# Performance work log

Measured on AMD Instinct MI355X. Metric: run time of the kernel, lower is better.

## Reference

```python
import jax, jax.numpy as jnp
import numpy as np
from jax import lax

DIM, HEADS, WS = 256, 8, 8
B, H, W = 2, 192, 192


def conv1x1(x, w, b):
    # x: (b,c,h,w), w: (o,c)
    return jnp.einsum('bchw,oc->bohw', x, w) + b[None, :, None, None]


def dwconv3x3(x, w, b):
    # w: (C,1,3,3), zeros padding (padding_mode='zeros')
    y = lax.conv_general_dilated(x, w, (1, 1), ((1, 1), (1, 1)),
                                 dimension_numbers=('NCHW', 'OIHW', 'NCHW'),
                                 feature_group_count=x.shape[1])
    return y + b[None, :, None, None]


def window_split(qkv):
    # (b, 3*heads*c, H, W) -> (3, b*h1*w1, heads, c, ws*ws)
    b, C3, h, w = qkv.shape
    c = C3 // (3 * HEADS)
    h1, w1 = h // WS, w // WS
    t = qkv.reshape(b, 3, HEADS, c, h1, WS, w1, WS)
    t = t.transpose(1, 0, 4, 6, 2, 3, 5, 7)  # (3,b,h1,w1,heads,c,ws,ws)
    return t.reshape(3, b * h1 * w1, HEADS, c, WS * WS)


def window_merge(o, b, h, w):
    # (b*h1*w1, heads, c, ws*ws) -> (b, heads*c, h, w)
    h1, w1 = h // WS, w // WS
    c = o.shape[2]
    t = o.reshape(b, h1, w1, HEADS, c, WS, WS)
    t = t.transpose(0, 3, 4, 1, 5, 2, 6)  # (b,heads,c,h1,ws,w1,ws)
    return t.reshape(b, HEADS * c, h, w)


def l2norm(x):
    n = jnp.linalg.norm(x, axis=-1, keepdims=True)
    return x / jnp.maximum(n, 1e-12)


def setup_inputs() -> dict:
    key = jax.random.key(0)
    ks = jax.random.split(key, 16)
    s = 0.02
    return {
        'x': jax.random.normal(ks[0], (B, DIM, H, W), jnp.float32),
        'x2': jax.random.normal(ks[1], (B, DIM, H, W), jnp.float32),
        'w_qkv': jax.random.normal(ks[2], (3 * DIM, DIM), jnp.float32) * s,
        'b_qkv': jnp.zeros((3 * DIM,), jnp.float32),
        'w_dw': jax.random.normal(ks[3], (3 * DIM, 1, 3, 3), jnp.float32) * s,
        'b_dw': jnp.zeros((3 * DIM,), jnp.float32),
        'w_qkv2': jax.random.normal(ks[4], (3 * DIM, DIM), jnp.float32) * s,
        'b_qkv2': jnp.zeros((3 * DIM,), jnp.float32),
        'w_dw2': jax.random.normal(ks[5], (3 * DIM, 1, 3, 3), jnp.float32) * s,
        'b_dw2': jnp.zeros((3 * DIM,), jnp.float32),
        'temp': jnp.ones((HEADS, 1, 1), jnp.float32) / np.sqrt(DIM).astype(np.float32),
        'w_proj': jax.random.normal(ks[6], (DIM, DIM), jnp.float32) * s,
        'b_proj': jnp.zeros((DIM,), jnp.float32),
    }


def reference(x, x2, w_qkv, b_qkv, w_dw, b_dw, w_qkv2, b_qkv2, w_dw2, b_dw2,
              temp, w_proj, b_proj):
    b, _, h, w = x.shape
    qkv = dwconv3x3(conv1x1(x, w_qkv, b_qkv), w_dw, b_dw)
    qkv2 = dwconv3x3(conv1x1(x2, w_qkv2, b_qkv2), w_dw2, b_dw2)
    # H,W divisible by window_size -> check_image_size is a no-op
    q, k, v = window_split(qkv)       # each (Bw, heads, c, N)
    q2, k2, v2 = window_split(qkv2)
    q, k = l2norm(q), l2norm(k)
    q2, k2 = l2norm(q2), l2norm(k2)
    # channel attention (cs='channel'): scores are (c x c) per window/head
    cross = jnp.einsum('whcn,whdn->whcd', q, k2) * temp  # q @ k2^T
    cross = jax.nn.softmax(cross, axis=-1)
    cross_out = jnp.einsum('whcd,whdn->whcn', cross, v2)
    out = window_merge(cross_out, b, h, w)
    return conv1x1(out, w_proj, b_proj)
```

## Files before the change

kernel.cpp:

```cpp
#include <hip/hip_runtime.h>
#include <stdint.h>

typedef unsigned short u16;
typedef __attribute__((ext_vector_type(4))) unsigned short u16x4;
typedef __attribute__((ext_vector_type(8))) short bf16x8;
typedef __attribute__((ext_vector_type(4))) float f32x4;

#define PTOT 36864
#define WIMG 192

__device__ __forceinline__ float bf2f(u16 h) {
    union { uint32_t u; float f; } v; v.u = ((uint32_t)h) << 16; return v.f;
}
__device__ __forceinline__ u16 f2bf(float f) {
    union { float f; uint32_t u; } v; v.f = f;
    uint32_t u = v.u;
    return (u16)((u + 0x7FFFu + ((u >> 16) & 1u)) >> 16);
}

#define ASYNC_COPY16(gp, lp)                                                     \
    __builtin_amdgcn_global_load_lds(                                            \
        (const __attribute__((address_space(1))) void*)(gp),                     \
        (__attribute__((address_space(3))) void*)(lp), 16, 0, 0)

__global__ __launch_bounds__(256) void k_transpose(const float* __restrict__ x,
                                                   u16* __restrict__ xt) {
    __shared__ u16 tile[32][33];
    const int tx = threadIdx.x, ty = threadIdx.y;
    const int p0 = blockIdx.x * 32, c0 = blockIdx.y * 32, b = blockIdx.z;
    const float* src = x + (size_t)b * 256 * PTOT;
    u16* dst = xt + (size_t)b * PTOT * 256;
#pragma unroll
    for (int k = 0; k < 4; ++k) {
        int c = c0 + ty + k * 8;
        tile[ty + k * 8][tx] = f2bf(src[(size_t)c * PTOT + p0 + tx]);
    }
    __syncthreads();
#pragma unroll
    for (int k = 0; k < 4; ++k) {
        int p = p0 + ty + k * 8;
        dst[(size_t)p * 256 + c0 + tx] = tile[tx][ty + k * 8];
    }
}

__global__ void k_f2bf(const float* __restrict__ src, u16* __restrict__ dst, int n) {
    int i = blockIdx.x * 256 + threadIdx.x;
    if (i < n) dst[i] = f2bf(src[i]);
}

template <bool OUT_F32>
__global__ __launch_bounds__(256) void k_gemm(const u16* __restrict__ A,
                                              const u16* __restrict__ Bt,
                                              void* __restrict__ Cout,
                                              const float* __restrict__ bias,
                                              int M) {
    __shared__ u16 As[128 * 32];
    __shared__ u16 Bs[128 * 32];
    const int tid = threadIdx.x;
    const int lane = tid & 63;
    const int wave = tid >> 6;
    const int wr = wave >> 1, wc = wave & 1;
    const int nb = blockIdx.x, mb = blockIdx.y, b = blockIdx.z;

    const u16* Ab = A + (size_t)(mb * 128) * 256;
    const u16* Bb = Bt + ((size_t)b * PTOT + (size_t)nb * 128) * 256;

    const int lrow = lane >> 2;
    const int lcol = (lane & 3) * 8;
    const int lr = lane & 15;
    const int lk = lane >> 4;

    f32x4 acc[4][4];
#pragma unroll
    for (int m = 0; m < 4; ++m)
#pragma unroll
        for (int n = 0; n < 4; ++n) acc[m][n] = (f32x4)0.f;

    for (int k0 = 0; k0 < 256; k0 += 32) {
        __syncthreads();
        const int i0 = wave * 2;
#pragma unroll
        for (int ii = 0; ii < 2; ++ii) {
            const int i = i0 + ii;
            ASYNC_COPY16(Ab + (size_t)(i * 16 + lrow) * 256 + k0 + lcol,
                         As + i * 16 * 32);
            ASYNC_COPY16(Bb + (size_t)(i * 16 + lrow) * 256 + k0 + lcol,
                         Bs + i * 16 * 32);
        }
        __syncthreads();
        const bf16x8* Asv = (const bf16x8*)As;
        const bf16x8* Bsv = (const bf16x8*)Bs;
        bf16x8 afr[4], bfr[4];
#pragma unroll
        for (int m = 0; m < 4; ++m)
            afr[m] = Asv[(wr * 64 + m * 16 + lr) * 4 + lk];
#pragma unroll
        for (int n = 0; n < 4; ++n)
            bfr[n] = Bsv[(wc * 64 + n * 16 + lr) * 4 + lk];
#pragma unroll
        for (int m = 0; m < 4; ++m)
#pragma unroll
            for (int n = 0; n < 4; ++n)
                acc[m][n] = __builtin_amdgcn_mfma_f32_16x16x32_bf16(
                    afr[m], bfr[n], acc[m][n], 0, 0, 0);
    }

    const int cr = (lane >> 4) * 4;
    const int cc = lane & 15;
#pragma unroll
    for (int m = 0; m < 4; ++m) {
#pragma unroll
        for (int j = 0; j < 4; ++j) {
            const int row = mb * 128 + wr * 64 + m * 16 + cr + j;
            const float bv = bias[row];
            const size_t rbase =
                ((size_t)b * M + row) * PTOT + (size_t)nb * 128 + wc * 64 + cc;
#pragma unroll
            for (int n = 0; n < 4; ++n) {
                const float v = acc[m][n][j] + bv;
                if (OUT_F32)
                    ((float*)Cout)[rbase + n * 16] = v;
                else
                    ((u16*)Cout)[rbase + n * 16] = f2bf(v);
            }
        }
    }
}

__global__ __launch_bounds__(256) void k_dwconv(const u16* __restrict__ in,
                                                u16* __restrict__ out,
                                                const float* __restrict__ w,
                                                const float* __restrict__ bias,
                                                int C) {
    const int vec = blockIdx.x * 256 + threadIdx.x;
    const int ch = blockIdx.y, b = blockIdx.z;
    const int yg = vec / 24, xv = vec - yg * 24;
    const int y0 = yg * 2;
    const size_t base = ((size_t)(b * C + ch)) * PTOT;
    const float* wc9 = w + ch * 9;

    float p[4][10];
#pragma unroll
    for (int r = 0; r < 4; ++r) {
        const int yy = y0 - 1 + r;
        if ((unsigned)yy >= (unsigned)WIMG) {
#pragma unroll
            for (int i = 0; i < 10; ++i) p[r][i] = 0.f;
        } else {
            const u16* row = in + base + (size_t)yy * WIMG + xv * 8;
            const bf16x8 cv = *(const bf16x8*)row;
            p[r][0] = (xv > 0) ? bf2f(row[-1]) : 0.f;
            p[r][9] = (xv < 23) ? bf2f(row[8]) : 0.f;
#pragma unroll
            for (int i = 0; i < 8; ++i) p[r][i + 1] = bf2f((u16)cv[i]);
        }
    }

    const float bv = bias[ch];
#pragma unroll
    for (int r = 0; r < 2; ++r) {
        float acc[8];
#pragma unroll
        for (int i = 0; i < 8; ++i) acc[i] = bv;
#pragma unroll
        for (int dy = 0; dy < 3; ++dy) {
            const float wa = wc9[dy * 3], wbv = wc9[dy * 3 + 1], wcv = wc9[dy * 3 + 2];
            const float* pr = p[r + dy];
#pragma unroll
            for (int i = 0; i < 8; ++i)
                acc[i] += wa * pr[i] + wbv * pr[i + 1] + wcv * pr[i + 2];
        }
        bf16x8 ov;
#pragma unroll
        for (int i = 0; i < 8; ++i) ov[i] = (short)f2bf(acc[i]);
        *(bf16x8*)(out + base + (size_t)(y0 + r) * WIMG + xv * 8) = ov;
    }
}

__global__ __launch_bounds__(256) void k_attn(const u16* __restrict__ q,
                                              const u16* __restrict__ kv,
                                              const float* __restrict__ temp,
                                              u16* __restrict__ outt) {
    __shared__ __align__(16) u16 lds[29280];
    u16* Q = lds;
    u16* K = lds + 9248;
    u16* VT = lds + 18496;
    float* IQ = (float*)(lds + 28768);
    float* IK = (float*)(lds + 29024);
    float* SS = (float*)(lds + 9248);
    u16* P = lds;

    const int tid = threadIdx.x;
    const int lane = tid & 63;
    const int wv = tid >> 6;
    const int h = blockIdx.y, b = blockIdx.z;
    const int wy = blockIdx.x / 6, wxg = blockIdx.x % 6;
    const int px0 = wxg * 32;

    const size_t qbase = ((size_t)b * 256 + h * 32) * PTOT;
    const size_t kbase = ((size_t)b * 512 + h * 32) * PTOT;
    const size_t vbase = kbase + (size_t)256 * PTOT;

#pragma unroll
    for (int it = 0; it < 4; ++it) {
        const int L = it * 256 + tid;
        const int c = L >> 5, rem = L & 31, rr = rem >> 2, w = rem & 3;
        const size_t gp = (size_t)(wy * 8 + rr) * WIMG + px0 + w * 8;
        bf16x8 qv = *(const bf16x8*)(q + qbase + (size_t)c * PTOT + gp);
        bf16x8 kvv = *(const bf16x8*)(kv + kbase + (size_t)c * PTOT + gp);
        bf16x8 vv = *(const bf16x8*)(kv + vbase + (size_t)c * PTOT + gp);
        *(bf16x8*)(Q + w * 2312 + c * 72 + rr * 8) = qv;
        *(bf16x8*)(K + w * 2312 + c * 72 + rr * 8) = kvv;
        u16* vt = VT + w * 2568 + rr * 8 * 40 + c;
#pragma unroll
        for (int j = 0; j < 8; ++j) vt[j * 40] = (u16)vv[j];
    }
    __syncthreads();

    {
        const int w = (tid >> 5) & 3, c = tid & 31;
        const u16* row = (tid < 128 ? Q : K) + w * 2312 + c * 72;
        float s = 0.f;
#pragma unroll
        for (int j = 0; j < 8; ++j) {
            bf16x8 v = *(const bf16x8*)(row + j * 8);
#pragma unroll
            for (int i = 0; i < 8; ++i) { float f = bf2f((u16)v[i]); s += f * f; }
        }
        const float inv = 1.f / fmaxf(sqrtf(s), 1e-12f);
        (tid < 128 ? IQ : IK)[w * 32 + c] = inv;
    }
    __syncthreads();

    {
        const int lr = lane & 15, lk = lane >> 4;
        f32x4 s00 = (f32x4)0.f, s01 = (f32x4)0.f, s10 = (f32x4)0.f, s11 = (f32x4)0.f;
        const u16* Qw = Q + wv * 2312 + lk * 8;
        const u16* Kw = K + wv * 2312 + lk * 8;
#pragma unroll
        for (int kb = 0; kb < 2; ++kb) {
            bf16x8 a0 = *(const bf16x8*)(Qw + lr * 72 + kb * 32);
            bf16x8 a1 = *(const bf16x8*)(Qw + (16 + lr) * 72 + kb * 32);
            bf16x8 b0 = *(const bf16x8*)(Kw + lr * 72 + kb * 32);
            bf16x8 b1 = *(const bf16x8*)(Kw + (16 + lr) * 72 + kb * 32);
            s00 = __builtin_amdgcn_mfma_f32_16x16x32_bf16(a0, b0, s00, 0, 0, 0);
            s01 = __builtin_amdgcn_mfma_f32_16x16x32_bf16(a0, b1, s01, 0, 0, 0);
            s10 = __builtin_amdgcn_mfma_f32_16x16x32_bf16(a1, b0, s10, 0, 0, 0);
            s11 = __builtin_amdgcn_mfma_f32_16x16x32_bf16(a1, b1, s11, 0, 0, 0);
        }
        float* srow = SS + wv * 1156;
        const int cr = lk * 4, cc = lr;
#pragma unroll
        for (int j = 0; j < 4; ++j) {
            srow[(cr + j) * 36 + cc] = s00[j];
            srow[(cr + j) * 36 + 16 + cc] = s01[j];
            srow[(16 + cr + j) * 36 + cc] = s10[j];
            srow[(16 + cr + j) * 36 + 16 + cc] = s11[j];
        }
    }
    __syncthreads();

    if (tid < 128) {
        const int w = tid >> 5, c = tid & 31;
        const float* srow = SS + w * 1156 + c * 36;
        const float* ik = IK + w * 32;
        const float iq = IQ[w * 32 + c] * temp[h];
        float sv[32];
        float mx = -1e30f;
#pragma unroll
        for (int d = 0; d < 32; ++d) {
            sv[d] = srow[d] * ik[d] * iq;
            mx = fmaxf(mx, sv[d]);
        }
        float sum = 0.f;
#pragma unroll
        for (int d = 0; d < 32; ++d) {
            sv[d] = __expf(sv[d] - mx);
            sum += sv[d];
        }
        const float inv = 1.f / sum;
        u16* prow = P + w * 2312 + c * 40;
#pragma unroll
        for (int ch = 0; ch < 4; ++ch) {
            bf16x8 pv;
#pragma unroll
            for (int i = 0; i < 8; ++i) pv[i] = (short)f2bf(sv[ch * 8 + i] * inv);
            *(bf16x8*)(prow + ch * 8) = pv;
        }
    }
    __syncthreads();

    {
        const int lr = lane & 15, lk = lane >> 4;
        bf16x8 pa0 = *(const bf16x8*)(P + wv * 2312 + lr * 40 + lk * 8);
        bf16x8 pa1 = *(const bf16x8*)(P + wv * 2312 + (16 + lr) * 40 + lk * 8);
        f32x4 o0[4], o1[4];
#pragma unroll
        for (int ni = 0; ni < 4; ++ni) { o0[ni] = (f32x4)0.f; o1[ni] = (f32x4)0.f; }
#pragma unroll
        for (int ni = 0; ni < 4; ++ni) {
            bf16x8 vb = *(const bf16x8*)(VT + wv * 2568 + (ni * 16 + lr) * 40 + lk * 8);
            o0[ni] = __builtin_amdgcn_mfma_f32_16x16x32_bf16(pa0, vb, o0[ni], 0, 0, 0);
            o1[ni] = __builtin_amdgcn_mfma_f32_16x16x32_bf16(pa1, vb, o1[ni], 0, 0, 0);
        }
#pragma unroll
        for (int ni = 0; ni < 4; ++ni) {
            const int n = ni * 16 + lr;
            const size_t gp = (size_t)(wy * 8 + (n >> 3)) * WIMG + px0 + wv * 8 + (n & 7);
            u16* op = outt + ((size_t)b * PTOT + gp) * 256 + h * 32;
            u16x4 pk0, pk1;
#pragma unroll
            for (int j = 0; j < 4; ++j) { pk0[j] = f2bf(o0[ni][j]); pk1[j] = f2bf(o1[ni][j]); }
            *(u16x4*)(op + lk * 4) = pk0;
            *(u16x4*)(op + 16 + lk * 4) = pk1;
        }
    }
}

extern "C" void kernel_launch(void* const* d_in, const int* in_sizes, int n_in,
                              void* d_out, int out_size, void* d_ws, size_t ws_size,
                              hipStream_t stream) {
    (void)in_sizes; (void)n_in; (void)out_size; (void)ws_size;
    const float* x      = (const float*)d_in[0];
    const float* x2     = (const float*)d_in[1];
    const float* w_qkv  = (const float*)d_in[2];
    const float* b_qkv  = (const float*)d_in[3];
    const float* w_dw   = (const float*)d_in[4];
    const float* b_dw   = (const float*)d_in[5];
    const float* w_qkv2 = (const float*)d_in[6];
    const float* b_qkv2 = (const float*)d_in[7];
    const float* w_dw2  = (const float*)d_in[8];
    const float* b_dw2  = (const float*)d_in[9];
    const float* temp   = (const float*)d_in[10];
    const float* w_proj = (const float*)d_in[11];
    const float* b_proj = (const float*)d_in[12];
    float* out = (float*)d_out;

    char* ws = (char*)d_ws;
    const size_t SZ_T  = (size_t)2 * PTOT * 256 * 2;
    const size_t SZ_KV = (size_t)2 * PTOT * 512 * 2;
    u16* xt     = (u16*)(ws);
    u16* x2t    = (u16*)(ws + SZ_T);
    u16* qpre   = (u16*)(ws + 2 * SZ_T);
    u16* kvpre  = (u16*)(ws + 3 * SZ_T);
    u16* kvconv = (u16*)(ws + 3 * SZ_T + SZ_KV);
    u16* wq     = (u16*)(ws + 3 * SZ_T + 2 * SZ_KV);
    u16* wkv    = wq + 256 * 256;
    u16* wproj  = wkv + 512 * 256;
    u16* qconv  = xt;
    u16* attnt  = x2t;

    const dim3 tb(32, 8);
    k_transpose<<<dim3(PTOT / 32, 8, 2), tb, 0, stream>>>(x, xt);
    k_transpose<<<dim3(PTOT / 32, 8, 2), tb, 0, stream>>>(x2, x2t);
    k_f2bf<<<(256 * 256 + 255) / 256, 256, 0, stream>>>(w_qkv, wq, 256 * 256);
    k_f2bf<<<(512 * 256 + 255) / 256, 256, 0, stream>>>(w_qkv2 + 256 * 256, wkv, 512 * 256);
    k_f2bf<<<(256 * 256 + 255) / 256, 256, 0, stream>>>(w_proj, wproj, 256 * 256);

    k_gemm<false><<<dim3(PTOT / 128, 2, 2), 256, 0, stream>>>(wq, xt, qpre, b_qkv, 256);
    k_gemm<false><<<dim3(PTOT / 128, 4, 2), 256, 0, stream>>>(wkv, x2t, kvpre, b_qkv2 + 256, 512);

    k_dwconv<<<dim3(2304 / 256, 256, 2), 256, 0, stream>>>(qpre, qconv, w_dw, b_dw, 256);
    k_dwconv<<<dim3(2304 / 256, 512, 2), 256, 0, stream>>>(kvpre, kvconv, w_dw2 + 256 * 9, b_dw2 + 256, 512);

    k_attn<<<dim3(144, 8, 2), 256, 0, stream>>>(qconv, kvconv, temp, attnt);

    k_gemm<true><<<dim3(PTOT / 128, 2, 2), 256, 0, stream>>>(wproj, attnt, out, b_proj, 256);
}
```

Measured before the change: 246.9 us.

## Load Q/K directly into MFMA registers, swizzle V^T LDS, widen transpose tiles, fuse weight casts

The attention kernel now loads Q and K straight from global memory into MFMA operand registers and computes the L2 norms with wave shuffles. This removes the Q/K LDS staging and one barrier, which shrinks LDS use and should allow more blocks per CU. The V^T layout in LDS is XOR-swizzled to reduce bank conflicts, and the score matrix stride changes from 36 to 33. The input transpose uses 64x64 tiles and the three weight bf16 conversions are merged into one launch. In exchange, the softmax stage gains an extra barrier because P now aliases the SS score buffer.

```diff
diff --git a/kernel.cpp b/kernel.cpp
--- a/kernel.cpp
+++ b/kernel.cpp
@@ -25,27 +25,34 @@
 
 __global__ __launch_bounds__(256) void k_transpose(const float* __restrict__ x,
                                                    u16* __restrict__ xt) {
-    __shared__ u16 tile[32][33];
+    __shared__ u16 tile[64][66];
     const int tx = threadIdx.x, ty = threadIdx.y;
-    const int p0 = blockIdx.x * 32, c0 = blockIdx.y * 32, b = blockIdx.z;
+    const int p0 = blockIdx.x * 64, c0 = blockIdx.y * 64, b = blockIdx.z;
     const float* src = x + (size_t)b * 256 * PTOT;
     u16* dst = xt + (size_t)b * PTOT * 256;
 #pragma unroll
-    for (int k = 0; k < 4; ++k) {
-        int c = c0 + ty + k * 8;
-        tile[ty + k * 8][tx] = f2bf(src[(size_t)c * PTOT + p0 + tx]);
-    }
-    __syncthreads();
-#pragma unroll
-    for (int k = 0; k < 4; ++k) {
-        int p = p0 + ty + k * 8;
-        dst[(size_t)p * 256 + c0 + tx] = tile[tx][ty + k * 8];
-    }
-}
-
-__global__ void k_f2bf(const float* __restrict__ src, u16* __restrict__ dst, int n) {
-    int i = blockIdx.x * 256 + threadIdx.x;
-    if (i < n) dst[i] = f2bf(src[i]);
+    for (int k = 0; k < 16; ++k) {
+        const int c = c0 + ty + k * 4;
+        tile[ty + k * 4][tx] = f2bf(src[(size_t)c * PTOT + p0 + tx]);
+    }
+    __syncthreads();
+#pragma unroll
+    for (int k = 0; k < 16; ++k) {
+        const int p = p0 + ty + k * 4;
+        dst[(size_t)p * 256 + c0 + tx] = tile[tx][ty + k * 4];
+    }
+}
+
+__global__ void k_f2bfAll(const float* __restrict__ w_qkv,
+                          const float* __restrict__ w_qkv2,
+                          const float* __restrict__ w_proj,
+                          u16* __restrict__ dst) {
+    const int i = blockIdx.x * 256 + threadIdx.x;
+    float v;
+    if (i < 65536) v = w_qkv[i];
+    else if (i < 196608) v = w_qkv2[i];
+    else v = w_proj[i - 196608];
+    dst[i] = f2bf(v);
 }
 
 template <bool OUT_F32>
@@ -181,14 +188,12 @@
                                               const u16* __restrict__ kv,
                                               const float* __restrict__ temp,
                                               u16* __restrict__ outt) {
-    __shared__ __align__(16) u16 lds[29280];
-    u16* Q = lds;
-    u16* K = lds + 9248;
-    u16* VT = lds + 18496;
-    float* IQ = (float*)(lds + 28768);
-    float* IK = (float*)(lds + 29024);
-    float* SS = (float*)(lds + 9248);
-    u16* P = lds;
+    __shared__ __align__(16) u16 lds[19232];
+    u16* VT = lds;
+    float* SS = (float*)(lds + 10272);
+    u16* P = lds + 10272;
+    float* IQ = (float*)(lds + 18720);
+    float* IK = (float*)(lds + 18976);
 
     const int tid = threadIdx.x;
     const int lane = tid & 63;
@@ -196,76 +201,89 @@
     const int h = blockIdx.y, b = blockIdx.z;
     const int wy = blockIdx.x / 6, wxg = blockIdx.x % 6;
     const int px0 = wxg * 32;
+    const int lr = lane & 15, lk = lane >> 4;
 
     const size_t qbase = ((size_t)b * 256 + h * 32) * PTOT;
     const size_t kbase = ((size_t)b * 512 + h * 32) * PTOT;
     const size_t vbase = kbase + (size_t)256 * PTOT;
+
+    bf16x8 aq[2][2], bk[2][2];
+#pragma unroll
+    for (int kb = 0; kb < 2; ++kb) {
+        const int rloc = kb * 4 + lk;
+        const size_t gp = (size_t)(wy * 8 + rloc) * WIMG + px0 + wv * 8;
+#pragma unroll
+        for (int half = 0; half < 2; ++half) {
+            const int ch = half * 16 + lr;
+            aq[kb][half] = *(const bf16x8*)(q + qbase + (size_t)ch * PTOT + gp);
+            bk[kb][half] = *(const bf16x8*)(kv + kbase + (size_t)ch * PTOT + gp);
+        }
+    }
+
+    {
+        float sq0 = 0.f, sq1 = 0.f, sk0 = 0.f, sk1 = 0.f;
+#pragma unroll
+        for (int kb = 0; kb < 2; ++kb)
+#pragma unroll
+            for (int j = 0; j < 8; ++j) {
+                float a0 = bf2f((u16)aq[kb][0][j]), a1 = bf2f((u16)aq[kb][1][j]);
+                float k0 = bf2f((u16)bk[kb][0][j]), k1 = bf2f((u16)bk[kb][1][j]);
+                sq0 += a0 * a0; sq1 += a1 * a1;
+                sk0 += k0 * k0; sk1 += k1 * k1;
+            }
+        sq0 += __shfl_xor(sq0, 16); sq0 += __shfl_xor(sq0, 32);
+        sq1 += __shfl_xor(sq1, 16); sq1 += __shfl_xor(sq1, 32);
+        sk0 += __shfl_xor(sk0, 16); sk0 += __shfl_xor(sk0, 32);
+        sk1 += __shfl_xor(sk1, 16); sk1 += __shfl_xor(sk1, 32);
+        if (lk == 0) {
+            IQ[wv * 32 + lr]      = 1.f / fmaxf(sqrtf(sq0), 1e-12f);
+            IQ[wv * 32 + 16 + lr] = 1.f / fmaxf(sqrtf(sq1), 1e-12f);
+            IK[wv * 32 + lr]      = 1.f / fmaxf(sqrtf(sk0), 1e-12f);
+            IK[wv * 32 + 16 + lr] = 1.f / fmaxf(sqrtf(sk1), 1e-12f);
+        }
+    }
 
 #pragma unroll
     for (int it = 0; it < 4; ++it) {
         const int L = it * 256 + tid;
         const int c = L >> 5, rem = L & 31, rr = rem >> 2, w = rem & 3;
         const size_t gp = (size_t)(wy * 8 + rr) * WIMG + px0 + w * 8;
-        bf16x8 qv = *(const bf16x8*)(q + qbase + (size_t)c * PTOT + gp);
-        bf16x8 kvv = *(const bf16x8*)(kv + kbase + (size_t)c * PTOT + gp);
         bf16x8 vv = *(const bf16x8*)(kv + vbase + (size_t)c * PTOT + gp);
-        *(bf16x8*)(Q + w * 2312 + c * 72 + rr * 8) = qv;
-        *(bf16x8*)(K + w * 2312 + c * 72 + rr * 8) = kvv;
-        u16* vt = VT + w * 2568 + rr * 8 * 40 + c;
+        const int blk = (c >> 3) ^ (rr & 3);
+        u16* vt = VT + w * 2568 + (rr * 8) * 40 + blk * 8 + (c & 7);
 #pragma unroll
         for (int j = 0; j < 8; ++j) vt[j * 40] = (u16)vv[j];
     }
     __syncthreads();
 
     {
-        const int w = (tid >> 5) & 3, c = tid & 31;
-        const u16* row = (tid < 128 ? Q : K) + w * 2312 + c * 72;
-        float s = 0.f;
-#pragma unroll
-        for (int j = 0; j < 8; ++j) {
-            bf16x8 v = *(const bf16x8*)(row + j * 8);
-#pragma unroll
-            for (int i = 0; i < 8; ++i) { float f = bf2f((u16)v[i]); s += f * f; }
-        }
-        const float inv = 1.f / fmaxf(sqrtf(s), 1e-12f);
-        (tid < 128 ? IQ : IK)[w * 32 + c] = inv;
-    }
-    __syncthreads();
-
-    {
-        const int lr = lane & 15, lk = lane >> 4;
         f32x4 s00 = (f32x4)0.f, s01 = (f32x4)0.f, s10 = (f32x4)0.f, s11 = (f32x4)0.f;
-        const u16* Qw = Q + wv * 2312 + lk * 8;
-        const u16* Kw = K + wv * 2312 + lk * 8;
 #pragma unroll
         for (int kb = 0; kb < 2; ++kb) {
-            bf16x8 a0 = *(const bf16x8*)(Qw + lr * 72 + kb * 32);
-            bf16x8 a1 = *(const bf16x8*)(Qw + (16 + lr) * 72 + kb * 32);
-            bf16x8 b0 = *(const bf16x8*)(Kw + lr * 72 + kb * 32);
-            bf16x8 b1 = *(const bf16x8*)(Kw + (16 + lr) * 72 + kb * 32);
-            s00 = __builtin_amdgcn_mfma_f32_16x16x32_bf16(a0, b0, s00, 0, 0, 0);
-            s01 = __builtin_amdgcn_mfma_f32_16x16x32_bf16(a0, b1, s01, 0, 0, 0);
-            s10 = __builtin_amdgcn_mfma_f32_16x16x32_bf16(a1, b0, s10, 0, 0, 0);
-            s11 = __builtin_amdgcn_mfma_f32_16x16x32_bf16(a1, b1, s11, 0, 0, 0);
-        }
-        float* srow = SS + wv * 1156;
+            s00 = __builtin_amdgcn_mfma_f32_16x16x32_bf16(aq[kb][0], bk[kb][0], s00, 0, 0, 0);
+            s01 = __builtin_amdgcn_mfma_f32_16x16x32_bf16(aq[kb][0], bk[kb][1], s01, 0, 0, 0);
+            s10 = __builtin_amdgcn_mfma_f32_16x16x32_bf16(aq[kb][1], bk[kb][0], s10, 0, 0, 0);
+            s11 = __builtin_amdgcn_mfma_f32_16x16x32_bf16(aq[kb][1], bk[kb][1], s11, 0, 0, 0);
+        }
+        float* srow = SS + wv * 1056;
         const int cr = lk * 4, cc = lr;
 #pragma unroll
         for (int j = 0; j < 4; ++j) {
-            srow[(cr + j) * 36 + cc] = s00[j];
-            srow[(cr + j) * 36 + 16 + cc] = s01[j];
-            srow[(16 + cr + j) * 36 + cc] = s10[j];
-            srow[(16 + cr + j) * 36 + 16 + cc] = s11[j];
-        }
-    }
-    __syncthreads();
-
+            srow[(cr + j) * 33 + cc] = s00[j];
+            srow[(cr + j) * 33 + 16 + cc] = s01[j];
+            srow[(16 + cr + j) * 33 + cc] = s10[j];
+            srow[(16 + cr + j) * 33 + 16 + cc] = s11[j];
+        }
+    }
+    __syncthreads();
+
+    float sv[32];
+    float pinv = 0.f;
+    const int sw = tid >> 5, sc = tid & 31;
     if (tid < 128) {
-        const int w = tid >> 5, c = tid & 31;
-        const float* srow = SS + w * 1156 + c * 36;
-        const float* ik = IK + w * 32;
-        const float iq = IQ[w * 32 + c] * temp[h];
-        float sv[32];
+        const float* srow = SS + sw * 1056 + sc * 33;
+        const float* ik = IK + sw * 32;
+        const float iq = IQ[sw * 32 + sc] * temp[h];
         float mx = -1e30f;
 #pragma unroll
         for (int d = 0; d < 32; ++d) {
@@ -278,28 +296,32 @@
             sv[d] = __expf(sv[d] - mx);
             sum += sv[d];
         }
-        const float inv = 1.f / sum;
-        u16* prow = P + w * 2312 + c * 40;
+        pinv = 1.f / sum;
+    }
+    __syncthreads();
+    if (tid < 128) {
+        u16* prow = P + sw * 1280 + sc * 40;
 #pragma unroll
         for (int ch = 0; ch < 4; ++ch) {
             bf16x8 pv;
 #pragma unroll
-            for (int i = 0; i < 8; ++i) pv[i] = (short)f2bf(sv[ch * 8 + i] * inv);
+            for (int i = 0; i < 8; ++i) pv[i] = (short)f2bf(sv[ch * 8 + i] * pinv);
             *(bf16x8*)(prow + ch * 8) = pv;
         }
     }
     __syncthreads();
 
     {
-        const int lr = lane & 15, lk = lane >> 4;
-        bf16x8 pa0 = *(const bf16x8*)(P + wv * 2312 + lr * 40 + lk * 8);
-        bf16x8 pa1 = *(const bf16x8*)(P + wv * 2312 + (16 + lr) * 40 + lk * 8);
+        bf16x8 pa0 = *(const bf16x8*)(P + wv * 1280 + lr * 40 + lk * 8);
+        bf16x8 pa1 = *(const bf16x8*)(P + wv * 1280 + (16 + lr) * 40 + lk * 8);
         f32x4 o0[4], o1[4];
 #pragma unroll
         for (int ni = 0; ni < 4; ++ni) { o0[ni] = (f32x4)0.f; o1[ni] = (f32x4)0.f; }
 #pragma unroll
         for (int ni = 0; ni < 4; ++ni) {
-            bf16x8 vb = *(const bf16x8*)(VT + wv * 2568 + (ni * 16 + lr) * 40 + lk * 8);
+            const int n = ni * 16 + lr;
+            const int blkr = lk ^ ((ni * 2 + (lr >> 3)) & 3);
+            bf16x8 vb = *(const bf16x8*)(VT + wv * 2568 + n * 40 + blkr * 8);
             o0[ni] = __builtin_amdgcn_mfma_f32_16x16x32_bf16(pa0, vb, o0[ni], 0, 0, 0);
             o1[ni] = __builtin_amdgcn_mfma_f32_16x16x32_bf16(pa1, vb, o1[ni], 0, 0, 0);
         }
@@ -350,12 +372,10 @@
     u16* qconv  = xt;
     u16* attnt  = x2t;
 
-    const dim3 tb(32, 8);
-    k_transpose<<<dim3(PTOT / 32, 8, 2), tb, 0, stream>>>(x, xt);
-    k_transpose<<<dim3(PTOT / 32, 8, 2), tb, 0, stream>>>(x2, x2t);
-    k_f2bf<<<(256 * 256 + 255) / 256, 256, 0, stream>>>(w_qkv, wq, 256 * 256);
-    k_f2bf<<<(512 * 256 + 255) / 256, 256, 0, stream>>>(w_qkv2 + 256 * 256, wkv, 512 * 256);
-    k_f2bf<<<(256 * 256 + 255) / 256, 256, 0, stream>>>(w_proj, wproj, 256 * 256);
+    const dim3 tb(64, 4);
+    k_transpose<<<dim3(PTOT / 64, 4, 2), tb, 0, stream>>>(x, xt);
+    k_transpose<<<dim3(PTOT / 64, 4, 2), tb, 0, stream>>>(x2, x2t);
+    k_f2bfAll<<<262144 / 256, 256, 0, stream>>>(w_qkv, w_qkv2, w_proj, wq);
 
     k_gemm<false><<<dim3(PTOT / 128, 2, 2), 256, 0, stream>>>(wq, xt, qpre, b_qkv, 256);
     k_gemm<false><<<dim3(PTOT / 128, 4, 2), 256, 0, stream>>>(wkv, x2t, kvpre, b_qkv2 + 256, 512);
```

After: 241.1 us. 1.02x faster.
